# Kernel tuning notes

Hardware: AMD Instinct MI355X
Metric: run time of the kernel (lower is better)

The kernel has to match this reference:

```python
import jax, jax.numpy as jnp
import numpy as np


def setup_inputs() -> dict:
    key = jax.random.key(0)
    ks = jax.random.split(key, 7)
    B, S, D_in, D_out, Q, K = 4, 1024, 256, 64, 128, 6
    X0 = jax.random.normal(ks[0], (B, S, D_in), dtype=jnp.float32)
    t = jax.random.uniform(ks[1], (B, 1), dtype=jnp.float32)
    Wc_w = jax.random.normal(ks[2], (Q, D_in), dtype=jnp.float32)
    Wc_b = jax.random.normal(ks[3], (Q,), dtype=jnp.float32)
    w = jax.random.normal(ks[4], (Q,), dtype=jnp.float32)
    A = jax.random.normal(ks[5], (D_out, Q, K), dtype=jnp.float32) / np.sqrt(Q * K)
    Bp = jax.random.uniform(ks[6], (D_out, Q, K), dtype=jnp.float32) * (2.0 * np.pi)
    return {"X0": X0, "t": t, "Wc_w": Wc_w, "Wc_b": Wc_b, "w": w, "A": A, "Bp": Bp}


def reference(X0, t, Wc_w, Wc_b, w, A, Bp):
    # C = Linear(X0): [B,S,Q]
    C = jnp.einsum('bsi,qi->bsq', X0, Wc_w) + Wc_b
    K = A.shape[-1]
    k_vec = jnp.arange(1, K + 1, dtype=X0.dtype)  # [K]
    # angle = C + w*t broadcast over S: [B,S,Q]
    angle = C + (w[None, :] * t)[:, None, :]
    # inner = angle*k + B : [B,S,D_out,Q,K]
    inner = angle[:, :, None, :, None] * k_vec + Bp[None, None]
    # V = sum over (Q,K) of A * sin(inner): [B,S,D_out]
    V = jnp.einsum('dqk,bsdqk->bsd', A, jnp.sin(inner))
    return V
```

## Files before the change

### kernel.cpp

```cpp
#include <hip/hip_runtime.h>
#include <math.h>

#define NB   4
#define NS   1024
#define DIN  256
#define DOUT 64
#define NQ   128
#define NK   6
#define NROW (NB*NS)
#define NF   (NQ*NK*2)
#define ROWS 16
#define THR  1024

#define W2T_OFF 0
#define WCH_OFF (DOUT*NF)
#define WCL_OFF (DOUT*NF + NQ*DIN)

typedef __attribute__((ext_vector_type(8))) short  short8;
typedef __attribute__((ext_vector_type(4))) short  short4v;
typedef __attribute__((ext_vector_type(4))) float  f32x4;

static __device__ __forceinline__ unsigned short f2bf(float x) {
    unsigned int u = __float_as_uint(x);
    u = (u + 0x7fffu + ((u >> 16) & 1u)) >> 16;
    return (unsigned short)u;
}
static __device__ __forceinline__ float bf2f(unsigned short h) {
    return __uint_as_float(((unsigned int)h) << 16);
}

__global__ __launch_bounds__(256) void k0_prep(const float* __restrict__ A,
                                               const float* __restrict__ Bp,
                                               const float* __restrict__ Wcw,
                                               unsigned short* __restrict__ ws) {
    int idx = blockIdx.x * 256 + threadIdx.x;
    if (idx < DOUT * NQ * NK) {
        int d   = idx / (NQ * NK);
        int rem = idx - d * (NQ * NK);
        int q   = rem / NK;
        int k   = rem - q * NK;
        float a = A[idx], bp = Bp[idx];
        float sb, cb;
        __sincosf(bp, &sb, &cb);
        ws[W2T_OFF + (size_t)d * NF + (k * 2 + 0) * NQ + q] = f2bf(a * cb);
        ws[W2T_OFF + (size_t)d * NF + (k * 2 + 1) * NQ + q] = f2bf(a * sb);
    } else {
        int j = idx - DOUT * NQ * NK;
        if (j < NQ * DIN) {
            float x = Wcw[j];
            unsigned short h = f2bf(x);
            unsigned short l = f2bf(x - bf2f(h));
            ws[WCH_OFF + j] = h;
            ws[WCL_OFF + j] = l;
        }
    }
}

__global__ __launch_bounds__(THR) void k_main(const float* __restrict__ X0,
                                              const float* __restrict__ tvec,
                                              const float* __restrict__ Wcb,
                                              const float* __restrict__ wq,
                                              const unsigned short* __restrict__ ws,
                                              float* __restrict__ V) {
    __shared__ char smem[65536];
    const int row0 = blockIdx.x * ROWS;
    const int tid  = threadIdx.x;
    const int lane = tid & 63;
    const int w    = tid >> 6;

    {
        const int r  = tid >> 6;
        const int kk = (tid & 63) * 4;
        float4 x = *(const float4*)(X0 + (size_t)(row0 + r) * DIN + kk);
        unsigned short h0 = f2bf(x.x), h1 = f2bf(x.y), h2 = f2bf(x.z), h3 = f2bf(x.w);
        short4v hv = {(short)h0, (short)h1, (short)h2, (short)h3};
        short4v lv = {(short)f2bf(x.x - bf2f(h0)), (short)f2bf(x.y - bf2f(h1)),
                      (short)f2bf(x.z - bf2f(h2)), (short)f2bf(x.w - bf2f(h3))};
        int off = (r * 512 + kk * 2) ^ ((r & 7) << 4);
        *(short4v*)(smem + off)        = hv;
        *(short4v*)(smem + 8192 + off) = lv;
    }
    __syncthreads();

    const int qt  = w & 7;
    const int kh  = w >> 3;
    const int col = lane & 15;
    const int kg  = lane >> 4;
    const int q   = qt * 16 + col;

    f32x4 acc = {0.f, 0.f, 0.f, 0.f};
    {
        const short8* bh = (const short8*)(ws + WCH_OFF + (size_t)q * DIN + kh * 128 + kg * 8);
        const short8* bl = (const short8*)(ws + WCL_OFF + (size_t)q * DIN + kh * 128 + kg * 8);
        const int asw = (col & 7) << 4;
        #pragma unroll
        for (int s = 0; s < 4; ++s) {
            int k    = kh * 128 + s * 32 + kg * 8;
            int aoff = (col * 512 + k * 2) ^ asw;
            short8 ah  = *(const short8*)(smem + aoff);
            short8 al  = *(const short8*)(smem + 8192 + aoff);
            short8 bhv = bh[s * 4];
            short8 blv = bl[s * 4];
            acc = __builtin_amdgcn_mfma_f32_16x16x32_bf16(ah, bhv, acc, 0, 0, 0);
            acc = __builtin_amdgcn_mfma_f32_16x16x32_bf16(ah, blv, acc, 0, 0, 0);
            acc = __builtin_amdgcn_mfma_f32_16x16x32_bf16(al, bhv, acc, 0, 0, 0);
        }
    }
    f32x4* R2A = (f32x4*)(smem + 49152);
    if (kh == 1) R2A[qt * 64 + lane] = acc;
    __syncthreads();

    if (kh == 0) {
        f32x4 p = R2A[qt * 64 + lane];
        const int   b    = row0 >> 10;
        const float bias = Wcb[q] + wq[q] * tvec[b];
        #pragma unroll
        for (int j = 0; j < 4; ++j) {
            float a = acc[j] + p[j] + bias;
            int   r = kg * 4 + j;
            int   sw = (r & 7) << 4;
            char* base = smem + r * (NF * 2);
            float s1, c1;
            __sincosf(a, &s1, &c1);
            float sk = s1, ck = c1;
            *(unsigned short*)(base + (((0 * NQ + q) * 2) ^ sw)) = f2bf(sk);
            *(unsigned short*)(base + (((1 * NQ + q) * 2) ^ sw)) = f2bf(ck);
            #pragma unroll
            for (int k = 1; k < NK; ++k) {
                float sn = sk * c1 + ck * s1;
                float cn = ck * c1 - sk * s1;
                *(unsigned short*)(base + ((((k * 2 + 0) * NQ + q) * 2) ^ sw)) = f2bf(sn);
                *(unsigned short*)(base + ((((k * 2 + 1) * NQ + q) * 2) ^ sw)) = f2bf(cn);
                sk = sn; ck = cn;
            }
        }
    }
    __syncthreads();

    const int dt  = w & 3;
    const int kq  = w >> 2;
    const int asw = (col & 7) << 4;
    f32x4 c2 = {0.f, 0.f, 0.f, 0.f};
    const unsigned short* wb = ws + W2T_OFF + (size_t)(dt * 16 + col) * NF + kg * 8;
    #pragma unroll 4
    for (int kk = 0; kk < 12; ++kk) {
        int k0   = kq * 384 + kk * 32;
        int aoff = (col * (NF * 2) + (k0 + kg * 8) * 2) ^ asw;
        short8 af = *(const short8*)(smem + aoff);
        short8 bf = *(const short8*)(wb + k0);
        c2 = __builtin_amdgcn_mfma_f32_16x16x32_bf16(af, bf, c2, 0, 0, 0);
    }
    f32x4* R4 = (f32x4*)(smem + 49152);
    if (kq != 0) R4[(kq * 4 + dt) * 64 + lane] = c2;
    __syncthreads();
    if (kq == 0) {
        c2 += R4[(1 * 4 + dt) * 64 + lane];
        c2 += R4[(2 * 4 + dt) * 64 + lane];
        c2 += R4[(3 * 4 + dt) * 64 + lane];
        const int d = dt * 16 + col;
        #pragma unroll
        for (int j = 0; j < 4; ++j)
            V[(size_t)(row0 + kg * 4 + j) * DOUT + d] = c2[j];
    }
}

extern "C" void kernel_launch(void* const* d_in, const int* in_sizes, int n_in,
                              void* d_out, int out_size, void* d_ws, size_t ws_size,
                              hipStream_t stream) {
    const float* X0   = (const float*)d_in[0];
    const float* tvec = (const float*)d_in[1];
    const float* Wcw  = (const float*)d_in[2];
    const float* Wcb  = (const float*)d_in[3];
    const float* wq   = (const float*)d_in[4];
    const float* A    = (const float*)d_in[5];
    const float* Bp   = (const float*)d_in[6];
    float*       V    = (float*)d_out;

    unsigned short* ws = (unsigned short*)d_ws;

    k0_prep<<<(DOUT * NQ * NK + NQ * DIN + 255) / 256, 256, 0, stream>>>(A, Bp, Wcw, ws);
    k_main <<<NROW / ROWS, THR, 0, stream>>>(X0, tvec, Wcb, wq, ws, V);
}
```

Before: 22.13 us.

## Fuse weight prep into main kernel with grid-wide flag synchronization

New measurement: 38.42 us. 1.74x slower.

```diff
diff --git a/kernel.cpp b/kernel.cpp
--- a/kernel.cpp
+++ b/kernel.cpp
@@ -11,10 +11,8 @@
 #define NF   (NQ*NK*2)
 #define ROWS 16
 #define THR  1024
-
-#define W2T_OFF 0
-#define WCH_OFF (DOUT*NF)
-#define WCL_OFF (DOUT*NF + NQ*DIN)
+#define NBLK (NROW/ROWS)
+#define MAGIC 0x1357A5A5u
 
 typedef __attribute__((ext_vector_type(8))) short  short8;
 typedef __attribute__((ext_vector_type(4))) short  short4v;
@@ -29,38 +27,15 @@
     return __uint_as_float(((unsigned int)h) << 16);
 }
 
-__global__ __launch_bounds__(256) void k0_prep(const float* __restrict__ A,
-                                               const float* __restrict__ Bp,
-                                               const float* __restrict__ Wcw,
-                                               unsigned short* __restrict__ ws) {
-    int idx = blockIdx.x * 256 + threadIdx.x;
-    if (idx < DOUT * NQ * NK) {
-        int d   = idx / (NQ * NK);
-        int rem = idx - d * (NQ * NK);
-        int q   = rem / NK;
-        int k   = rem - q * NK;
-        float a = A[idx], bp = Bp[idx];
-        float sb, cb;
-        __sincosf(bp, &sb, &cb);
-        ws[W2T_OFF + (size_t)d * NF + (k * 2 + 0) * NQ + q] = f2bf(a * cb);
-        ws[W2T_OFF + (size_t)d * NF + (k * 2 + 1) * NQ + q] = f2bf(a * sb);
-    } else {
-        int j = idx - DOUT * NQ * NK;
-        if (j < NQ * DIN) {
-            float x = Wcw[j];
-            unsigned short h = f2bf(x);
-            unsigned short l = f2bf(x - bf2f(h));
-            ws[WCH_OFF + j] = h;
-            ws[WCL_OFF + j] = l;
-        }
-    }
-}
-
 __global__ __launch_bounds__(THR) void k_main(const float* __restrict__ X0,
                                               const float* __restrict__ tvec,
+                                              const float* __restrict__ Wcw,
                                               const float* __restrict__ Wcb,
                                               const float* __restrict__ wq,
-                                              const unsigned short* __restrict__ ws,
+                                              const float* __restrict__ A,
+                                              const float* __restrict__ Bp,
+                                              unsigned short* __restrict__ W2T,
+                                              unsigned int* __restrict__ flags,
                                               float* __restrict__ V) {
     __shared__ char smem[65536];
     const int row0 = blockIdx.x * ROWS;
@@ -68,10 +43,24 @@
     const int lane = tid & 63;
     const int w    = tid >> 6;
 
+    const int r  = w;
+    const int kk = lane * 4;
+    float4 x = *(const float4*)(X0 + (size_t)(row0 + r) * DIN + kk);
+
+    if (tid < 192) {
+        int e   = blockIdx.x * 192 + tid;
+        int d   = e / (NQ * NK);
+        int rem = e - d * (NQ * NK);
+        int q   = rem / NK;
+        int k   = rem - q * NK;
+        float a = A[e], bp = Bp[e];
+        float sb, cb;
+        __sincosf(bp, &sb, &cb);
+        W2T[(size_t)d * NF + (k * 2 + 0) * NQ + q] = f2bf(a * cb);
+        W2T[(size_t)d * NF + (k * 2 + 1) * NQ + q] = f2bf(a * sb);
+    }
+
     {
-        const int r  = tid >> 6;
-        const int kk = (tid & 63) * 4;
-        float4 x = *(const float4*)(X0 + (size_t)(row0 + r) * DIN + kk);
         unsigned short h0 = f2bf(x.x), h1 = f2bf(x.y), h2 = f2bf(x.z), h3 = f2bf(x.w);
         short4v hv = {(short)h0, (short)h1, (short)h2, (short)h3};
         short4v lv = {(short)f2bf(x.x - bf2f(h0)), (short)f2bf(x.y - bf2f(h1)),
@@ -82,44 +71,58 @@
     }
     __syncthreads();
 
+    if (tid == 0) {
+        __threadfence();
+        __hip_atomic_store(&flags[blockIdx.x], MAGIC,
+                           __ATOMIC_RELAXED, __HIP_MEMORY_SCOPE_AGENT);
+    }
+
     const int qt  = w & 7;
     const int kh  = w >> 3;
     const int col = lane & 15;
     const int kg  = lane >> 4;
     const int q   = qt * 16 + col;
+    const int asw = (col & 7) << 4;
 
     f32x4 acc = {0.f, 0.f, 0.f, 0.f};
     {
-        const short8* bh = (const short8*)(ws + WCH_OFF + (size_t)q * DIN + kh * 128 + kg * 8);
-        const short8* bl = (const short8*)(ws + WCL_OFF + (size_t)q * DIN + kh * 128 + kg * 8);
-        const int asw = (col & 7) << 4;
+        const float* wrow = Wcw + (size_t)q * DIN + kh * 128 + kg * 8;
         #pragma unroll
         for (int s = 0; s < 4; ++s) {
             int k    = kh * 128 + s * 32 + kg * 8;
             int aoff = (col * 512 + k * 2) ^ asw;
-            short8 ah  = *(const short8*)(smem + aoff);
-            short8 al  = *(const short8*)(smem + 8192 + aoff);
-            short8 bhv = bh[s * 4];
-            short8 blv = bl[s * 4];
-            acc = __builtin_amdgcn_mfma_f32_16x16x32_bf16(ah, bhv, acc, 0, 0, 0);
-            acc = __builtin_amdgcn_mfma_f32_16x16x32_bf16(ah, blv, acc, 0, 0, 0);
-            acc = __builtin_amdgcn_mfma_f32_16x16x32_bf16(al, bhv, acc, 0, 0, 0);
+            short8 ah = *(const short8*)(smem + aoff);
+            short8 al = *(const short8*)(smem + 8192 + aoff);
+            float4 w0 = *(const float4*)(wrow + s * 32);
+            float4 w1 = *(const float4*)(wrow + s * 32 + 4);
+            float wf[8] = {w0.x, w0.y, w0.z, w0.w, w1.x, w1.y, w1.z, w1.w};
+            short8 bh, bl;
+            #pragma unroll
+            for (int j = 0; j < 8; ++j) {
+                unsigned short h = f2bf(wf[j]);
+                bh[j] = (short)h;
+                bl[j] = (short)f2bf(wf[j] - bf2f(h));
+            }
+            acc = __builtin_amdgcn_mfma_f32_16x16x32_bf16(ah, bh, acc, 0, 0, 0);
+            acc = __builtin_amdgcn_mfma_f32_16x16x32_bf16(ah, bl, acc, 0, 0, 0);
+            acc = __builtin_amdgcn_mfma_f32_16x16x32_bf16(al, bh, acc, 0, 0, 0);
         }
     }
+
     f32x4* R2A = (f32x4*)(smem + 49152);
-    if (kh == 1) R2A[qt * 64 + lane] = acc;
+    R2A[(kh * 8 + qt) * 64 + lane] = acc;
     __syncthreads();
-
-    if (kh == 0) {
-        f32x4 p = R2A[qt * 64 + lane];
+    {
+        f32x4 other = R2A[((1 - kh) * 8 + qt) * 64 + lane];
         const int   b    = row0 >> 10;
         const float bias = Wcb[q] + wq[q] * tvec[b];
         #pragma unroll
-        for (int j = 0; j < 4; ++j) {
-            float a = acc[j] + p[j] + bias;
-            int   r = kg * 4 + j;
-            int   sw = (r & 7) << 4;
-            char* base = smem + r * (NF * 2);
+        for (int jj = 0; jj < 2; ++jj) {
+            int   j  = kh * 2 + jj;
+            float a  = acc[j] + other[j] + bias;
+            int   rr = kg * 4 + j;
+            int   sw = (rr & 7) << 4;
+            char* base = smem + rr * (NF * 2);
             float s1, c1;
             __sincosf(a, &s1, &c1);
             float sk = s1, ck = c1;
@@ -137,14 +140,21 @@
     }
     __syncthreads();
 
-    const int dt  = w & 3;
-    const int kq  = w >> 2;
-    const int asw = (col & 7) << 4;
+    if (tid < NBLK) {
+        while (__hip_atomic_load(&flags[tid], __ATOMIC_RELAXED,
+                                 __HIP_MEMORY_SCOPE_AGENT) != MAGIC)
+            __builtin_amdgcn_s_sleep(2);
+        __threadfence();
+    }
+    __syncthreads();
+
+    const int dt = w & 3;
+    const int kq = w >> 2;
     f32x4 c2 = {0.f, 0.f, 0.f, 0.f};
-    const unsigned short* wb = ws + W2T_OFF + (size_t)(dt * 16 + col) * NF + kg * 8;
+    const unsigned short* wb = W2T + (size_t)(dt * 16 + col) * NF + kg * 8;
     #pragma unroll 4
-    for (int kk = 0; kk < 12; ++kk) {
-        int k0   = kq * 384 + kk * 32;
+    for (int kt = 0; kt < 12; ++kt) {
+        int k0   = kq * 384 + kt * 32;
         int aoff = (col * (NF * 2) + (k0 + kg * 8) * 2) ^ asw;
         short8 af = *(const short8*)(smem + aoff);
         short8 bf = *(const short8*)(wb + k0);
@@ -176,8 +186,9 @@
     const float* Bp   = (const float*)d_in[6];
     float*       V    = (float*)d_out;
 
-    unsigned short* ws = (unsigned short*)d_ws;
+    unsigned short* W2T   = (unsigned short*)d_ws;
+    unsigned int*   flags = (unsigned int*)((char*)d_ws + 196608);
 
-    k0_prep<<<(DOUT * NQ * NK + NQ * DIN + 255) / 256, 256, 0, stream>>>(A, Bp, Wcw, ws);
-    k_main <<<NROW / ROWS, THR, 0, stream>>>(X0, tvec, Wcb, wq, ws, V);
+    k_main<<<NBLK, THR, 0, stream>>>(X0, tvec, Wcw, Wcb, wq, A, Bp,
+                                     W2T, flags, V);
 }
```
